# Kernel optimization log

Hardware: AMD Instinct MI355X
Metric: run time of the kernel (lower is better)

Reference implementation:

```python
import jax, jax.numpy as jnp
import numpy as np

N, E, DIN, DOUT = 40000, 640000, 128, 10


def _gat_layer(h_in, src, dst, W, a_src, a_dst, b, n_nodes):
    # h: [N, D]; edges include self-loops already
    h = h_in @ W
    alpha = jax.nn.leaky_relu((h @ a_src)[src] + (h @ a_dst)[dst], 0.2)  # [E']
    m = jax.ops.segment_max(alpha, dst, num_segments=n_nodes)
    e = jnp.exp(alpha - m[dst])
    s = jax.ops.segment_sum(e, dst, num_segments=n_nodes)
    coef = e / (s[dst] + 1e-16)
    out = jax.ops.segment_sum(h[src] * coef[:, None], dst, num_segments=n_nodes)
    return out + b


def setup_inputs() -> dict:
    key = jax.random.key(0)
    ks = jax.random.split(key, 20)
    p = lambda k, shp: (jax.random.normal(k, shp, dtype=jnp.float32) * 0.05)
    inp = {
        "x": jax.random.normal(ks[0], (N, DIN), dtype=jnp.float32),
        "edge_index": jax.random.randint(ks[1], (2, E), 0, N, dtype=jnp.int32),
        "batch": jnp.sort(jax.random.randint(ks[2], (N,), 0, 64, dtype=jnp.int32)),
        "edge_attr": jax.random.normal(ks[3], (E, 4), dtype=jnp.float32),
        # GATConv 1: 128 -> 64
        "W1": p(ks[4], (DIN, 64)), "a1s": p(ks[5], (64,)), "a1d": p(ks[6], (64,)), "b1": jnp.zeros((64,), jnp.float32),
        # GATConv 2: 64 -> 128
        "W2": p(ks[7], (64, 128)), "a2s": p(ks[8], (128,)), "a2d": p(ks[9], (128,)), "b2": jnp.zeros((128,), jnp.float32),
        # GATConv 3: 128 -> 128
        "W3": p(ks[10], (128, 128)), "a3s": p(ks[11], (128,)), "a3d": p(ks[12], (128,)), "b3": jnp.zeros((128,), jnp.float32),
        # SAGPooling scorer: GraphConv(128, 1)
        "wp_rel": p(ks[13], (128, 1)), "wp_root": p(ks[14], (128, 1)), "bp": jnp.zeros((1,), jnp.float32),
        # final Linear(128, out_channels)
        "Wl": p(ks[15], (128, DOUT)), "bl": jnp.zeros((DOUT,), jnp.float32),
    }
    return inp


def reference(x, edge_index, batch, edge_attr,
              W1, a1s, a1d, b1, W2, a2s, a2d, b2, W3, a3s, a3d, b3,
              wp_rel, wp_root, bp, Wl, bl):
    n = x.shape[0]
    src, dst = edge_index[0], edge_index[1]
    # GATConv adds self-loops (edge_attr unused: edge_dim=None)
    loops = jnp.arange(n, dtype=src.dtype)
    src_sl = jnp.concatenate([src, loops])
    dst_sl = jnp.concatenate([dst, loops])

    h = jax.nn.relu(_gat_layer(x, src_sl, dst_sl, W1, a1s, a1d, b1, n))
    h = jax.nn.relu(_gat_layer(h, src_sl, dst_sl, W2, a2s, a2d, b2, n))
    h = jax.nn.relu(_gat_layer(h, src_sl, dst_sl, W3, a3s, a3d, b3, n))

    # SAGPooling(ratio=1): score via GraphConv (no self-loops), tanh gating, all nodes kept
    agg = jax.ops.segment_sum(h[src], dst, num_segments=n)  # [N, 128]
    score = (agg @ wp_rel + h @ wp_root + bp)[:, 0]         # [N]
    h = h * jnp.tanh(score)[:, None]

    # dropout is identity in eval mode
    return jax.nn.relu(h @ Wl + bl)
```

## Files before the change

### kernel.cpp

```cpp
#include <hip/hip_runtime.h>
#include <math.h>

template<int K, int N>
__global__ __launch_bounds__(128) void gemm_rt(
    const float* __restrict__ A, const float* __restrict__ B,
    float* __restrict__ C, int M,
    const float* __restrict__ va, const float* __restrict__ vb,
    float* __restrict__ outa, float* __restrict__ outb)
{
    constexpr int KC = 32;
    constexpr int NC = K / KC;
    constexpr int TC = N / 8;
    constexpr int TR = 128 / TC;
    constexpr int MR = 64 / TR;
    constexpr int KT = KC / TC;
    constexpr int AST = 68;

    __shared__ float AsT[KC * AST];
    __shared__ float Bs[KC * N];

    const int tid = threadIdx.x;
    const int base = blockIdx.x * 64;
    const int tc = tid % TC;
    const int tr = tid / TC;
    const int sq = tid & 7;
    const int sr = tid >> 3;

    float acc[MR][8];
#pragma unroll
    for (int m = 0; m < MR; ++m)
#pragma unroll
        for (int j = 0; j < 8; ++j) acc[m][j] = 0.f;
    float sa[MR], sb[MR];
#pragma unroll
    for (int m = 0; m < MR; ++m) { sa[m] = 0.f; sb[m] = 0.f; }

    for (int ch = 0; ch < NC; ++ch) {
        const int k0 = ch * KC;
#pragma unroll
        for (int rr = sr; rr < 64; rr += 16) {
            int gr = base + rr;
            float4 av = (gr < M) ? *(const float4*)(A + (size_t)gr * K + k0 + 4 * sq)
                                 : make_float4(0.f, 0.f, 0.f, 0.f);
            AsT[(4 * sq + 0) * AST + rr] = av.x;
            AsT[(4 * sq + 1) * AST + rr] = av.y;
            AsT[(4 * sq + 2) * AST + rr] = av.z;
            AsT[(4 * sq + 3) * AST + rr] = av.w;
        }
#pragma unroll
        for (int t = tid; t < KC * N / 4; t += 128) {
            int f = t * 4;
            int k = f / N, c = f % N;
            *(float4*)(Bs + k * N + c) = *(const float4*)(B + (size_t)(k0 + k) * N + c);
        }
        __syncthreads();

#pragma unroll 4
        for (int kk = 0; kk < KC; ++kk) {
            const float* ap = AsT + kk * AST + MR * tr;
            const float* bp = Bs + kk * N + 8 * tc;
            float4 b0 = *(const float4*)(bp);
            float4 b1 = *(const float4*)(bp + 4);
            float4 a0 = *(const float4*)(ap);
#pragma unroll
            for (int m = 0; m < 4; ++m) {
                float av = ((const float*)&a0)[m];
                acc[m][0] = fmaf(av, b0.x, acc[m][0]);
                acc[m][1] = fmaf(av, b0.y, acc[m][1]);
                acc[m][2] = fmaf(av, b0.z, acc[m][2]);
                acc[m][3] = fmaf(av, b0.w, acc[m][3]);
                acc[m][4] = fmaf(av, b1.x, acc[m][4]);
                acc[m][5] = fmaf(av, b1.y, acc[m][5]);
                acc[m][6] = fmaf(av, b1.z, acc[m][6]);
                acc[m][7] = fmaf(av, b1.w, acc[m][7]);
            }
            if constexpr (MR == 8) {
                float4 a1 = *(const float4*)(ap + 4);
#pragma unroll
                for (int m = 0; m < 4; ++m) {
                    float av = ((const float*)&a1)[m];
                    acc[m + 4][0] = fmaf(av, b0.x, acc[m + 4][0]);
                    acc[m + 4][1] = fmaf(av, b0.y, acc[m + 4][1]);
                    acc[m + 4][2] = fmaf(av, b0.z, acc[m + 4][2]);
                    acc[m + 4][3] = fmaf(av, b0.w, acc[m + 4][3]);
                    acc[m + 4][4] = fmaf(av, b1.x, acc[m + 4][4]);
                    acc[m + 4][5] = fmaf(av, b1.y, acc[m + 4][5]);
                    acc[m + 4][6] = fmaf(av, b1.z, acc[m + 4][6]);
                    acc[m + 4][7] = fmaf(av, b1.w, acc[m + 4][7]);
                }
            }
        }
        if (va != nullptr) {
#pragma unroll
            for (int kl = 0; kl < KT; ++kl) {
                int k = tc * KT + kl;
                float av_ = va[k0 + k];
                float bv_ = vb[k0 + k];
#pragma unroll
                for (int m = 0; m < MR; ++m) {
                    float aval = AsT[k * AST + MR * tr + m];
                    sa[m] = fmaf(aval, av_, sa[m]);
                    sb[m] = fmaf(aval, bv_, sb[m]);
                }
            }
        }
        __syncthreads();
    }

#pragma unroll
    for (int m = 0; m < MR; ++m) {
        int gr = base + MR * tr + m;
        if (gr < M) {
            float4 o0 = make_float4(acc[m][0], acc[m][1], acc[m][2], acc[m][3]);
            float4 o1 = make_float4(acc[m][4], acc[m][5], acc[m][6], acc[m][7]);
            *(float4*)(C + (size_t)gr * N + 8 * tc) = o0;
            *(float4*)(C + (size_t)gr * N + 8 * tc + 4) = o1;
        }
    }
    if (va != nullptr) {
#pragma unroll
        for (int m = 0; m < MR; ++m) {
#pragma unroll
            for (int off = TC / 2; off; off >>= 1) {
                sa[m] += __shfl_xor(sa[m], off);
                sb[m] += __shfl_xor(sb[m], off);
            }
        }
        if (tc == 0) {
#pragma unroll
            for (int m = 0; m < MR; ++m) {
                int gr = base + MR * tr + m;
                if (gr < M) { outa[gr] = sa[m]; outb[gr] = sb[m]; }
            }
        }
    }
}

template<int K, int N, int NT>
__global__ __launch_bounds__(256) void gemm_tile(
    const float* __restrict__ A, const float* __restrict__ B,
    float* __restrict__ C, int M,
    const float* __restrict__ bias, const float* __restrict__ score, int outN)
{
    __shared__ float As[64 * K];
    const int tid = threadIdx.x;
    const int base = blockIdx.x * 64;
    for (int idx = tid; idx < 64 * K; idx += 256) {
        int r = idx / K, k = idx - r * K;
        int gr = base + r;
        As[idx] = (gr < M) ? A[(size_t)gr * K + k] : 0.f;
    }
    __syncthreads();
    constexpr int RSTEP = 256 / NT;
    constexpr int NR = 64 / RSTEP;
    const int c = tid % NT;
    const int r0 = tid / NT;
    float acc[NR];
#pragma unroll
    for (int i = 0; i < NR; ++i) acc[i] = 0.f;
    const float4* As4 = reinterpret_cast<const float4*>(As);
    const float* Bc = B + c;
    float b0 = Bc[0 * N], b1 = Bc[1 * N], b2 = Bc[2 * N], b3 = Bc[3 * N];
    for (int k = 0; k < K; k += 4) {
        const int kn = (k + 4 < K) ? (k + 4) : k;
        float n0 = Bc[(kn + 0) * N];
        float n1 = Bc[(kn + 1) * N];
        float n2 = Bc[(kn + 2) * N];
        float n3 = Bc[(kn + 3) * N];
#pragma unroll
        for (int i = 0; i < NR; ++i) {
            float4 a = As4[((r0 + i * RSTEP) * K + k) >> 2];
            acc[i] = fmaf(a.x, b0, acc[i]);
            acc[i] = fmaf(a.y, b1, acc[i]);
            acc[i] = fmaf(a.z, b2, acc[i]);
            acc[i] = fmaf(a.w, b3, acc[i]);
        }
        b0 = n0; b1 = n1; b2 = n2; b3 = n3;
    }
    if (c < outN) {
#pragma unroll
        for (int i = 0; i < NR; ++i) {
            int gr = base + r0 + i * RSTEP;
            if (gr < M) {
                float v = tanhf(score[gr]) * acc[i] + bias[c];
                C[(size_t)gr * outN + c] = fmaxf(v, 0.f);
            }
        }
    }
}

__global__ __launch_bounds__(256) void hist_deg(
    const int* __restrict__ dst, int* __restrict__ deg, int E, int n)
{
    int e = blockIdx.x * 256 + threadIdx.x;
    if (e >= E + n) return;
    int d = (e < E) ? dst[e] : (e - E);
    atomicAdd(deg + d, 1);
}

__global__ __launch_bounds__(256) void scan_local(
    const int* __restrict__ deg, int* __restrict__ row_start, int* __restrict__ blocksum, int n)
{
    __shared__ int s[256];
    const int t = threadIdx.x;
    const int i = blockIdx.x * 256 + t;
    int v = (i < n) ? deg[i] : 0;
    s[t] = v;
    __syncthreads();
#pragma unroll
    for (int off = 1; off < 256; off <<= 1) {
        int u = (t >= off) ? s[t - off] : 0;
        __syncthreads();
        s[t] += u;
        __syncthreads();
    }
    if (i < n) row_start[i] = s[t] - v;
    if (t == 255) blocksum[blockIdx.x] = s[255];
}

__global__ __launch_bounds__(256) void scan_blocks(int* __restrict__ blocksum, int nb)
{
    __shared__ int s[256];
    const int t = threadIdx.x;
    int v = (t < nb) ? blocksum[t] : 0;
    s[t] = v;
    __syncthreads();
#pragma unroll
    for (int off = 1; off < 256; off <<= 1) {
        int u = (t >= off) ? s[t - off] : 0;
        __syncthreads();
        s[t] += u;
        __syncthreads();
    }
    if (t < nb) blocksum[t] = s[t] - v;
}

__global__ __launch_bounds__(256) void scan_add(
    int* __restrict__ row_start, int* __restrict__ cursor,
    const int* __restrict__ blocksum, int n, int total)
{
    const int i = blockIdx.x * 256 + threadIdx.x;
    if (i < n) {
        int v = row_start[i] + blocksum[blockIdx.x];
        row_start[i] = v;
        cursor[i] = v;
    } else if (i == n) {
        row_start[n] = total;
    }
}

__global__ __launch_bounds__(256) void fill_csr(
    const int* __restrict__ src, const int* __restrict__ dst,
    int* __restrict__ cursor, int* __restrict__ csr_src, int E, int n)
{
    int e = blockIdx.x * 256 + threadIdx.x;
    if (e >= E + n) return;
    int s, d;
    if (e < E) { s = src[e]; d = dst[e]; } else { s = d = e - E; }
    int pos = atomicAdd(cursor + d, 1);
    csr_src[pos] = s;
}

template<int D, bool POOL>
__global__ __launch_bounds__(256) void gat_aggregate(
    const int* __restrict__ row_start, const int* __restrict__ csr_src,
    const float* __restrict__ asv, const float* __restrict__ adv,
    const float* __restrict__ h, const float* __restrict__ bias,
    float* __restrict__ out,
    const float* __restrict__ wpr, const float* __restrict__ wpo,
    float* __restrict__ poolA, float* __restrict__ poolB, int n)
{
    __shared__ float lds_e[4][128];
    __shared__ int   lds_i[4][128];
    const int node = (blockIdx.x * 256 + threadIdx.x) >> 6;
    const int lane = threadIdx.x & 63;
    const int w = threadIdx.x >> 6;
    if (node >= n) return;
    const int beg = row_start[node];
    const int deg = row_start[node + 1] - beg;
    const float advv = adv[node];
    const bool fast = (deg <= 128);

    float amax = -INFINITY;
    if (fast) {
        for (int j = lane; j < deg; j += 64) {
            int s = csr_src[beg + j];
            lds_i[w][j] = s;
            float a = asv[s] + advv;
            a = (a >= 0.f) ? a : 0.2f * a;
            lds_e[w][j] = a;
            amax = fmaxf(amax, a);
        }
    } else {
        for (int j = lane; j < deg; j += 64) {
            float a = asv[csr_src[beg + j]] + advv;
            a = (a >= 0.f) ? a : 0.2f * a;
            amax = fmaxf(amax, a);
        }
    }
#pragma unroll
    for (int off = 32; off; off >>= 1) amax = fmaxf(amax, __shfl_xor(amax, off));

    float ssum = 0.f;
    if (fast) {
        for (int j = lane; j < deg; j += 64) {
            float ev = expf(lds_e[w][j] - amax);
            lds_e[w][j] = ev;
            ssum += ev;
        }
    } else {
        for (int j = lane; j < deg; j += 64) {
            float a = asv[csr_src[beg + j]] + advv;
            a = (a >= 0.f) ? a : 0.2f * a;
            ssum += expf(a - amax);
        }
    }
#pragma unroll
    for (int off = 32; off; off >>= 1) ssum += __shfl_xor(ssum, off);
    const float inv = 1.f / (ssum + 1e-16f);

    if (fast) {
        if constexpr (D == 128) {
            const float4* h4 = reinterpret_cast<const float4*>(h);
            const int half = lane >> 5;
            const int fl = lane & 31;
            float4 a0 = {0,0,0,0}, a1 = {0,0,0,0}, a2 = {0,0,0,0}, a3 = {0,0,0,0};
            int j = 0;
            for (; j + 8 <= deg; j += 8) {
                int e0 = j + half, e1 = j + 2 + half, e2 = j + 4 + half, e3 = j + 6 + half;
                int s0 = lds_i[w][e0], s1 = lds_i[w][e1], s2 = lds_i[w][e2], s3 = lds_i[w][e3];
                float c0 = lds_e[w][e0] * inv, c1 = lds_e[w][e1] * inv;
                float c2 = lds_e[w][e2] * inv, c3 = lds_e[w][e3] * inv;
                float4 v0 = h4[(size_t)s0 * 32 + fl];
                float4 v1 = h4[(size_t)s1 * 32 + fl];
                float4 v2 = h4[(size_t)s2 * 32 + fl];
                float4 v3 = h4[(size_t)s3 * 32 + fl];
                a0.x = fmaf(v0.x, c0, a0.x); a0.y = fmaf(v0.y, c0, a0.y);
                a0.z = fmaf(v0.z, c0, a0.z); a0.w = fmaf(v0.w, c0, a0.w);
                a1.x = fmaf(v1.x, c1, a1.x); a1.y = fmaf(v1.y, c1, a1.y);
                a1.z = fmaf(v1.z, c1, a1.z); a1.w = fmaf(v1.w, c1, a1.w);
                a2.x = fmaf(v2.x, c2, a2.x); a2.y = fmaf(v2.y, c2, a2.y);
                a2.z = fmaf(v2.z, c2, a2.z); a2.w = fmaf(v2.w, c2, a2.w);
                a3.x = fmaf(v3.x, c3, a3.x); a3.y = fmaf(v3.y, c3, a3.y);
                a3.z = fmaf(v3.z, c3, a3.z); a3.w = fmaf(v3.w, c3, a3.w);
            }
            for (; j < deg; j += 2) {
                int e = j + half;
                bool ok = (e < deg);
                int s = lds_i[w][ok ? e : 0];
                float c = ok ? lds_e[w][e] * inv : 0.f;
                float4 v = h4[(size_t)s * 32 + fl];
                a0.x = fmaf(v.x, c, a0.x); a0.y = fmaf(v.y, c, a0.y);
                a0.z = fmaf(v.z, c, a0.z); a0.w = fmaf(v.w, c, a0.w);
            }
            float4 t;
            t.x = (a0.x + a1.x) + (a2.x + a3.x);
            t.y = (a0.y + a1.y) + (a2.y + a3.y);
            t.z = (a0.z + a1.z) + (a2.z + a3.z);
            t.w = (a0.w + a1.w) + (a2.w + a3.w);
            t.x += __shfl_xor(t.x, 32);
            t.y += __shfl_xor(t.y, 32);
            t.z += __shfl_xor(t.z, 32);
            t.w += __shfl_xor(t.w, 32);
            const float4 b4 = reinterpret_cast<const float4*>(bias)[fl];
            float4 o;
            o.x = fmaxf(t.x + b4.x, 0.f);
            o.y = fmaxf(t.y + b4.y, 0.f);
            o.z = fmaxf(t.z + b4.z, 0.f);
            o.w = fmaxf(t.w + b4.w, 0.f);
            if (half == 0)
                reinterpret_cast<float4*>(out)[(size_t)node * 32 + fl] = o;
            if constexpr (POOL) {
                const float4 r4 = reinterpret_cast<const float4*>(wpr)[fl];
                const float4 q4 = reinterpret_cast<const float4*>(wpo)[fl];
                float pa = o.x * r4.x + o.y * r4.y + o.z * r4.z + o.w * r4.w;
                float pb = o.x * q4.x + o.y * q4.y + o.z * q4.z + o.w * q4.w;
#pragma unroll
                for (int off = 16; off; off >>= 1) {
                    pa += __shfl_xor(pa, off);
                    pb += __shfl_xor(pb, off);
                }
                if (lane == 0) { poolA[node] = pa; poolB[node] = pb; }
            }
        } else {
            const float4* h4 = reinterpret_cast<const float4*>(h);
            const int q = lane >> 4;
            const int fl = lane & 15;
            float4 a0 = {0,0,0,0}, a1 = {0,0,0,0};
            int j = 0;
            for (; j + 8 <= deg; j += 8) {
                int e0 = j + q, e1 = j + 4 + q;
                int s0 = lds_i[w][e0], s1 = lds_i[w][e1];
                float c0 = lds_e[w][e0] * inv, c1 = lds_e[w][e1] * inv;
                float4 v0 = h4[(size_t)s0 * 16 + fl];
                float4 v1 = h4[(size_t)s1 * 16 + fl];
                a0.x = fmaf(v0.x, c0, a0.x); a0.y = fmaf(v0.y, c0, a0.y);
                a0.z = fmaf(v0.z, c0, a0.z); a0.w = fmaf(v0.w, c0, a0.w);
                a1.x = fmaf(v1.x, c1, a1.x); a1.y = fmaf(v1.y, c1, a1.y);
                a1.z = fmaf(v1.z, c1, a1.z); a1.w = fmaf(v1.w, c1, a1.w);
            }
            for (; j < deg; j += 4) {
                int e = j + q;
                bool ok = (e < deg);
                int s = lds_i[w][ok ? e : 0];
                float c = ok ? lds_e[w][e] * inv : 0.f;
                float4 v = h4[(size_t)s * 16 + fl];
                a0.x = fmaf(v.x, c, a0.x); a0.y = fmaf(v.y, c, a0.y);
                a0.z = fmaf(v.z, c, a0.z); a0.w = fmaf(v.w, c, a0.w);
            }
            float4 t;
            t.x = a0.x + a1.x; t.y = a0.y + a1.y; t.z = a0.z + a1.z; t.w = a0.w + a1.w;
            t.x += __shfl_xor(t.x, 16); t.x += __shfl_xor(t.x, 32);
            t.y += __shfl_xor(t.y, 16); t.y += __shfl_xor(t.y, 32);
            t.z += __shfl_xor(t.z, 16); t.z += __shfl_xor(t.z, 32);
            t.w += __shfl_xor(t.w, 16); t.w += __shfl_xor(t.w, 32);
            const float4 b4 = reinterpret_cast<const float4*>(bias)[fl];
            float4 o;
            o.x = fmaxf(t.x + b4.x, 0.f);
            o.y = fmaxf(t.y + b4.y, 0.f);
            o.z = fmaxf(t.z + b4.z, 0.f);
            o.w = fmaxf(t.w + b4.w, 0.f);
            if (q == 0)
                reinterpret_cast<float4*>(out)[(size_t)node * 16 + fl] = o;
        }
    } else {
        if constexpr (D == 128) {
            const float2* h2 = reinterpret_cast<const float2*>(h);
            float2 a0 = {0.f, 0.f};
            for (int j = 0; j < deg; ++j) {
                int s = csr_src[beg + j];
                float a = asv[s] + advv;
                a = (a >= 0.f) ? a : 0.2f * a;
                float c = expf(a - amax) * inv;
                float2 v = h2[(size_t)s * 64 + lane];
                a0.x = fmaf(v.x, c, a0.x); a0.y = fmaf(v.y, c, a0.y);
            }
            float2 o;
            o.x = fmaxf(a0.x + bias[2 * lane], 0.f);
            o.y = fmaxf(a0.y + bias[2 * lane + 1], 0.f);
            reinterpret_cast<float2*>(out)[(size_t)node * 64 + lane] = o;
            if constexpr (POOL) {
                float pa = fmaf(o.x, wpr[2 * lane], o.y * wpr[2 * lane + 1]);
                float pb = fmaf(o.x, wpo[2 * lane], o.y * wpo[2 * lane + 1]);
#pragma unroll
                for (int off = 32; off; off >>= 1) {
                    pa += __shfl_xor(pa, off);
                    pb += __shfl_xor(pb, off);
                }
                if (lane == 0) { poolA[node] = pa; poolB[node] = pb; }
            }
        } else {
            float a0 = 0.f;
            for (int j = 0; j < deg; ++j) {
                int s = csr_src[beg + j];
                float a = asv[s] + advv;
                a = (a >= 0.f) ? a : 0.2f * a;
                float c = expf(a - amax) * inv;
                a0 = fmaf(h[(size_t)s * D + lane], c, a0);
            }
            out[(size_t)node * D + lane] = fmaxf(a0 + bias[lane], 0.f);
        }
    }
}

__global__ __launch_bounds__(256) void score_csr(
    const int* __restrict__ row_start, const int* __restrict__ csr_src,
    const float* __restrict__ ts, const float* __restrict__ td,
    const float* __restrict__ bp, float* __restrict__ score, int n)
{
    int i = blockIdx.x * 256 + threadIdx.x;
    if (i >= n) return;
    int beg = row_start[i], end = row_start[i + 1];
    float s = td[i] + bp[0] - ts[i];
    for (int j = beg; j < end; ++j) s += ts[csr_src[j]];
    score[i] = s;
}

__global__ __launch_bounds__(256) void precompute(
    const float* __restrict__ W1, const float* __restrict__ a1s, const float* __restrict__ a1d,
    const float* __restrict__ W2, const float* __restrict__ a2s, const float* __restrict__ a2d,
    const float* __restrict__ W3, const float* __restrict__ a3s, const float* __restrict__ a3d,
    const float* __restrict__ Wl, const float* __restrict__ bl,
    float* __restrict__ va1, float* __restrict__ vb1,
    float* __restrict__ va2, float* __restrict__ vb2,
    float* __restrict__ va3, float* __restrict__ vb3,
    float* __restrict__ Wlp, float* __restrict__ blp,
    int* __restrict__ deg, int n)
{
    int t = blockIdx.x * 256 + threadIdx.x;
    if (t < n) deg[t] = 0;
    if (t < 128) {
        float sa = 0.f, sb = 0.f;
        for (int j = 0; j < 64; ++j) {
            float w = W1[t * 64 + j];
            sa = fmaf(w, a1s[j], sa); sb = fmaf(w, a1d[j], sb);
        }
        va1[t] = sa; vb1[t] = sb;
    } else if (t < 192) {
        int k = t - 128;
        float sa = 0.f, sb = 0.f;
        for (int j = 0; j < 128; ++j) {
            float w = W2[k * 128 + j];
            sa = fmaf(w, a2s[j], sa); sb = fmaf(w, a2d[j], sb);
        }
        va2[k] = sa; vb2[k] = sb;
    } else if (t < 320) {
        int k = t - 192;
        float sa = 0.f, sb = 0.f;
        for (int j = 0; j < 128; ++j) {
            float w = W3[k * 128 + j];
            sa = fmaf(w, a3s[j], sa); sb = fmaf(w, a3d[j], sb);
        }
        va3[k] = sa; vb3[k] = sb;
    } else if (t < 320 + 2048) {
        int i = t - 320;
        int k = i >> 4, c = i & 15;
        Wlp[i] = (c < 10) ? Wl[k * 10 + c] : 0.f;
    } else if (t < 320 + 2048 + 16) {
        int c = t - (320 + 2048);
        blp[c] = (c < 10) ? bl[c] : 0.f;
    }
}

extern "C" void kernel_launch(void* const* d_in, const int* in_sizes, int n_in,
                              void* d_out, int out_size, void* d_ws, size_t ws_size,
                              hipStream_t stream) {
    const float* x   = (const float*)d_in[0];
    const int*   ei  = (const int*)d_in[1];
    const float* W1  = (const float*)d_in[4];
    const float* a1s = (const float*)d_in[5];
    const float* a1d = (const float*)d_in[6];
    const float* b1  = (const float*)d_in[7];
    const float* W2  = (const float*)d_in[8];
    const float* a2s = (const float*)d_in[9];
    const float* a2d = (const float*)d_in[10];
    const float* b2  = (const float*)d_in[11];
    const float* W3  = (const float*)d_in[12];
    const float* a3s = (const float*)d_in[13];
    const float* a3d = (const float*)d_in[14];
    const float* b3  = (const float*)d_in[15];
    const float* wpr = (const float*)d_in[16];
    const float* wpo = (const float*)d_in[17];
    const float* bp  = (const float*)d_in[18];
    const float* Wl  = (const float*)d_in[19];
    const float* bl  = (const float*)d_in[20];

    const int n = in_sizes[0] / 128;
    const int E = in_sizes[1] / 2;
    const int Esl = E + n;
    const int* src = ei;
    const int* dst = ei + E;

    float* ws = (float*)d_ws;
    const size_t nd = (size_t)n * 128;
    float* bufA      = ws;
    float* bufB      = bufA + nd;
    float* asv       = bufB + nd;
    float* adv       = asv + n;
    float* tsv       = adv + n;
    float* tdv       = tsv + n;
    float* score     = tdv + n;
    int*   deg       = (int*)(score + n);
    int*   row_start = deg + n;
    int*   cursor    = row_start + n + 1;
    int*   blocksum  = cursor + n;
    int*   csr_src   = blocksum + 256;
    float* va1       = (float*)(csr_src + Esl);
    float* vb1       = va1 + 128;
    float* va2       = vb1 + 128;
    float* vb2       = va2 + 64;
    float* va3       = vb2 + 64;
    float* vb3       = va3 + 128;
    float* Wlp       = vb3 + 128;
    float* blp       = Wlp + 128 * 16;

    const unsigned EB = (unsigned)((Esl + 255) / 256);
    const unsigned NB = (unsigned)((n + 255) / 256);
    const unsigned MB = (unsigned)((n + 63) / 64);
    const unsigned WB = (unsigned)(((size_t)n * 64 + 255) / 256);

    precompute<<<NB, 256, 0, stream>>>(W1, a1s, a1d, W2, a2s, a2d, W3, a3s, a3d, Wl, bl,
                                       va1, vb1, va2, vb2, va3, vb3, Wlp, blp, deg, n);
    hist_deg<<<EB, 256, 0, stream>>>(dst, deg, E, n);
    scan_local<<<NB, 256, 0, stream>>>(deg, row_start, blocksum, n);
    scan_blocks<<<1, 256, 0, stream>>>(blocksum, (int)NB);
    scan_add<<<NB, 256, 0, stream>>>(row_start, cursor, blocksum, n, Esl);
    fill_csr<<<EB, 256, 0, stream>>>(src, dst, cursor, csr_src, E, n);

    gemm_rt<128, 64><<<MB, 128, 0, stream>>>(x, W1, bufA, n, va1, vb1, asv, adv);
    gat_aggregate<64, false><<<WB, 256, 0, stream>>>(row_start, csr_src, asv, adv, bufA, b1, bufB,
                                                     nullptr, nullptr, nullptr, nullptr, n);

    gemm_rt<64, 128><<<MB, 128, 0, stream>>>(bufB, W2, bufA, n, va2, vb2, asv, adv);
    gat_aggregate<128, false><<<WB, 256, 0, stream>>>(row_start, csr_src, asv, adv, bufA, b2, bufB,
                                                      nullptr, nullptr, nullptr, nullptr, n);

    gemm_rt<128, 128><<<MB, 128, 0, stream>>>(bufB, W3, bufA, n, va3, vb3, asv, adv);
    gat_aggregate<128, true><<<WB, 256, 0, stream>>>(row_start, csr_src, asv, adv, bufA, b3, bufB,
                                                     wpr, wpo, tsv, tdv, n);

    score_csr<<<NB, 256, 0, stream>>>(row_start, csr_src, tsv, tdv, bp, score, n);
    gemm_tile<128, 16, 16><<<MB, 256, 0, stream>>>(bufB, Wlp, (float*)d_out, n, blp, score, 10);
}
```

Measured before the change: 332.0 us.

## Register-prefetch next K-chunk in gemm_rt and scale threads with output width

```diff
diff --git a/kernel.cpp b/kernel.cpp
--- a/kernel.cpp
+++ b/kernel.cpp
@@ -2,19 +2,23 @@
 #include <math.h>
 
 template<int K, int N>
-__global__ __launch_bounds__(128) void gemm_rt(
+__global__ __launch_bounds__(2 * N) void gemm_rt(
     const float* __restrict__ A, const float* __restrict__ B,
     float* __restrict__ C, int M,
-    const float* __restrict__ va, const float* __restrict__ vb,
-    float* __restrict__ outa, float* __restrict__ outb)
+    const float* __restrict__ iva, const float* __restrict__ ivb,
+    float* __restrict__ ioa, float* __restrict__ iob,
+    const float* __restrict__ ebias,
+    const float* __restrict__ eva, const float* __restrict__ evb,
+    float* __restrict__ eoa, float* __restrict__ eob)
 {
     constexpr int KC = 32;
     constexpr int NC = K / KC;
     constexpr int TC = N / 8;
-    constexpr int TR = 128 / TC;
-    constexpr int MR = 64 / TR;
+    constexpr int NT = 2 * N;
     constexpr int KT = KC / TC;
     constexpr int AST = 68;
+    constexpr int A_F4 = 512 / NT;
+    constexpr int B_F4 = 4;
 
     __shared__ float AsT[KC * AST];
     __shared__ float Bs[KC * N];
@@ -23,45 +27,69 @@
     const int base = blockIdx.x * 64;
     const int tc = tid % TC;
     const int tr = tid / TC;
-    const int sq = tid & 7;
-    const int sr = tid >> 3;
-
-    float acc[MR][8];
-#pragma unroll
-    for (int m = 0; m < MR; ++m)
+
+    float acc[4][8];
+#pragma unroll
+    for (int m = 0; m < 4; ++m)
 #pragma unroll
         for (int j = 0; j < 8; ++j) acc[m][j] = 0.f;
-    float sa[MR], sb[MR];
-#pragma unroll
-    for (int m = 0; m < MR; ++m) { sa[m] = 0.f; sb[m] = 0.f; }
+    float sa[4], sb[4];
+#pragma unroll
+    for (int m = 0; m < 4; ++m) { sa[m] = 0.f; sb[m] = 0.f; }
+
+    float4 ra[A_F4], rb[B_F4];
+
+#pragma unroll
+    for (int j = 0; j < A_F4; ++j) {
+        int i = tid + j * NT; int row = i >> 3; int q = i & 7;
+        int gr = base + row;
+        ra[j] = (gr < M) ? *(const float4*)(A + (size_t)gr * K + 4 * q)
+                         : make_float4(0.f, 0.f, 0.f, 0.f);
+    }
+#pragma unroll
+    for (int j = 0; j < B_F4; ++j) {
+        int i = tid + j * NT; int kk_ = i / (N / 4); int c4 = i % (N / 4);
+        rb[j] = *(const float4*)(B + (size_t)kk_ * N + 4 * c4);
+    }
 
     for (int ch = 0; ch < NC; ++ch) {
-        const int k0 = ch * KC;
-#pragma unroll
-        for (int rr = sr; rr < 64; rr += 16) {
-            int gr = base + rr;
-            float4 av = (gr < M) ? *(const float4*)(A + (size_t)gr * K + k0 + 4 * sq)
+#pragma unroll
+        for (int j = 0; j < A_F4; ++j) {
+            int i = tid + j * NT; int row = i >> 3; int q = i & 7;
+            AsT[(4 * q + 0) * AST + row] = ra[j].x;
+            AsT[(4 * q + 1) * AST + row] = ra[j].y;
+            AsT[(4 * q + 2) * AST + row] = ra[j].z;
+            AsT[(4 * q + 3) * AST + row] = ra[j].w;
+        }
+#pragma unroll
+        for (int j = 0; j < B_F4; ++j) {
+            int i = tid + j * NT; int kk_ = i / (N / 4); int c4 = i % (N / 4);
+            *(float4*)(Bs + kk_ * N + 4 * c4) = rb[j];
+        }
+        __syncthreads();
+
+        if (ch + 1 < NC) {
+            const int k0 = (ch + 1) * KC;
+#pragma unroll
+            for (int j = 0; j < A_F4; ++j) {
+                int i = tid + j * NT; int row = i >> 3; int q = i & 7;
+                int gr = base + row;
+                ra[j] = (gr < M) ? *(const float4*)(A + (size_t)gr * K + k0 + 4 * q)
                                  : make_float4(0.f, 0.f, 0.f, 0.f);
-            AsT[(4 * sq + 0) * AST + rr] = av.x;
-            AsT[(4 * sq + 1) * AST + rr] = av.y;
-            AsT[(4 * sq + 2) * AST + rr] = av.z;
-            AsT[(4 * sq + 3) * AST + rr] = av.w;
-        }
-#pragma unroll
-        for (int t = tid; t < KC * N / 4; t += 128) {
-            int f = t * 4;
-            int k = f / N, c = f % N;
-            *(float4*)(Bs + k * N + c) = *(const float4*)(B + (size_t)(k0 + k) * N + c);
-        }
-        __syncthreads();
-
-#pragma unroll 4
+            }
+#pragma unroll
+            for (int j = 0; j < B_F4; ++j) {
+                int i = tid + j * NT; int kk_ = i / (N / 4); int c4 = i % (N / 4);
+                rb[j] = *(const float4*)(B + (size_t)(k0 + kk_) * N + 4 * c4);
+            }
+        }
+
+#pragma unroll 8
         for (int kk = 0; kk < KC; ++kk) {
-            const float* ap = AsT + kk * AST + MR * tr;
+            float4 a0 = *(const float4*)(AsT + kk * AST + 4 * tr);
             const float* bp = Bs + kk * N + 8 * tc;
             float4 b0 = *(const float4*)(bp);
             float4 b1 = *(const float4*)(bp + 4);
-            float4 a0 = *(const float4*)(ap);
 #pragma unroll
             for (int m = 0; m < 4; ++m) {
                 float av = ((const float*)&a0)[m];
@@ -74,31 +102,18 @@
                 acc[m][6] = fmaf(av, b1.z, acc[m][6]);
                 acc[m][7] = fmaf(av, b1.w, acc[m][7]);
             }
-            if constexpr (MR == 8) {
-                float4 a1 = *(const float4*)(ap + 4);
-#pragma unroll
-                for (int m = 0; m < 4; ++m) {
-                    float av = ((const float*)&a1)[m];
-                    acc[m + 4][0] = fmaf(av, b0.x, acc[m + 4][0]);
-                    acc[m + 4][1] = fmaf(av, b0.y, acc[m + 4][1]);
-                    acc[m + 4][2] = fmaf(av, b0.z, acc[m + 4][2]);
-                    acc[m + 4][3] = fmaf(av, b0.w, acc[m + 4][3]);
-                    acc[m + 4][4] = fmaf(av, b1.x, acc[m + 4][4]);
-                    acc[m + 4][5] = fmaf(av, b1.y, acc[m + 4][5]);
-                    acc[m + 4][6] = fmaf(av, b1.z, acc[m + 4][6]);
-                    acc[m + 4][7] = fmaf(av, b1.w, acc[m + 4][7]);
-                }
-            }
-        }
-        if (va != nullptr) {
+        }
+
+        if (iva != nullptr) {
+            const int k0 = ch * KC;
 #pragma unroll
             for (int kl = 0; kl < KT; ++kl) {
                 int k = tc * KT + kl;
-                float av_ = va[k0 + k];
-                float bv_ = vb[k0 + k];
-#pragma unroll
-                for (int m = 0; m < MR; ++m) {
-                    float aval = AsT[k * AST + MR * tr + m];
+                float av_ = iva[k0 + k];
+                float bv_ = ivb[k0 + k];
+#pragma unroll
+                for (int m = 0; m < 4; ++m) {
+                    float aval = AsT[k * AST + 4 * tr + m];
                     sa[m] = fmaf(aval, av_, sa[m]);
                     sb[m] = fmaf(aval, bv_, sb[m]);
                 }
@@ -107,19 +122,51 @@
         __syncthreads();
     }
 
-#pragma unroll
-    for (int m = 0; m < MR; ++m) {
-        int gr = base + MR * tr + m;
+    float pa[4], pb[4];
+#pragma unroll
+    for (int m = 0; m < 4; ++m) { pa[m] = 0.f; pb[m] = 0.f; }
+#pragma unroll
+    for (int m = 0; m < 4; ++m) {
+        int gr = base + 4 * tr + m;
+        float o[8];
+#pragma unroll
+        for (int j = 0; j < 8; ++j) o[j] = acc[m][j];
+        if (ebias != nullptr) {
+#pragma unroll
+            for (int j = 0; j < 8; ++j) o[j] = fmaxf(o[j] + ebias[8 * tc + j], 0.f);
+        }
         if (gr < M) {
-            float4 o0 = make_float4(acc[m][0], acc[m][1], acc[m][2], acc[m][3]);
-            float4 o1 = make_float4(acc[m][4], acc[m][5], acc[m][6], acc[m][7]);
-            *(float4*)(C + (size_t)gr * N + 8 * tc) = o0;
-            *(float4*)(C + (size_t)gr * N + 8 * tc + 4) = o1;
-        }
-    }
-    if (va != nullptr) {
-#pragma unroll
-        for (int m = 0; m < MR; ++m) {
+            *(float4*)(C + (size_t)gr * N + 8 * tc) = make_float4(o[0], o[1], o[2], o[3]);
+            *(float4*)(C + (size_t)gr * N + 8 * tc + 4) = make_float4(o[4], o[5], o[6], o[7]);
+        }
+        if (eva != nullptr) {
+#pragma unroll
+            for (int j = 0; j < 8; ++j) {
+                pa[m] = fmaf(o[j], eva[8 * tc + j], pa[m]);
+                pb[m] = fmaf(o[j], evb[8 * tc + j], pb[m]);
+            }
+        }
+    }
+    if (eva != nullptr) {
+#pragma unroll
+        for (int m = 0; m < 4; ++m) {
+#pragma unroll
+            for (int off = TC / 2; off; off >>= 1) {
+                pa[m] += __shfl_xor(pa[m], off);
+                pb[m] += __shfl_xor(pb[m], off);
+            }
+        }
+        if (tc == 0) {
+#pragma unroll
+            for (int m = 0; m < 4; ++m) {
+                int gr = base + 4 * tr + m;
+                if (gr < M) { eoa[gr] = pa[m]; eob[gr] = pb[m]; }
+            }
+        }
+    }
+    if (iva != nullptr) {
+#pragma unroll
+        for (int m = 0; m < 4; ++m) {
 #pragma unroll
             for (int off = TC / 2; off; off >>= 1) {
                 sa[m] += __shfl_xor(sa[m], off);
@@ -128,9 +175,9 @@
         }
         if (tc == 0) {
 #pragma unroll
-            for (int m = 0; m < MR; ++m) {
-                int gr = base + MR * tr + m;
-                if (gr < M) { outa[gr] = sa[m]; outb[gr] = sb[m]; }
+            for (int m = 0; m < 4; ++m) {
+                int gr = base + 4 * tr + m;
+                if (gr < M) { ioa[gr] = sa[m]; iob[gr] = sb[m]; }
             }
         }
     }
@@ -587,15 +634,18 @@
     scan_add<<<NB, 256, 0, stream>>>(row_start, cursor, blocksum, n, Esl);
     fill_csr<<<EB, 256, 0, stream>>>(src, dst, cursor, csr_src, E, n);
 
-    gemm_rt<128, 64><<<MB, 128, 0, stream>>>(x, W1, bufA, n, va1, vb1, asv, adv);
+    gemm_rt<128, 64><<<MB, 128, 0, stream>>>(
+        x, W1, bufA, n, va1, vb1, asv, adv, nullptr, nullptr, nullptr, nullptr, nullptr);
     gat_aggregate<64, false><<<WB, 256, 0, stream>>>(row_start, csr_src, asv, adv, bufA, b1, bufB,
                                                      nullptr, nullptr, nullptr, nullptr, n);
 
-    gemm_rt<64, 128><<<MB, 128, 0, stream>>>(bufB, W2, bufA, n, va2, vb2, asv, adv);
+    gemm_rt<64, 128><<<MB, 256, 0, stream>>>(
+        bufB, W2, bufA, n, va2, vb2, asv, adv, nullptr, nullptr, nullptr, nullptr, nullptr);
     gat_aggregate<128, false><<<WB, 256, 0, stream>>>(row_start, csr_src, asv, adv, bufA, b2, bufB,
                                                       nullptr, nullptr, nullptr, nullptr, n);
 
-    gemm_rt<128, 128><<<MB, 128, 0, stream>>>(bufB, W3, bufA, n, va3, vb3, asv, adv);
+    gemm_rt<128, 128><<<MB, 256, 0, stream>>>(
+        bufB, W3, bufA, n, va3, vb3, asv, adv, nullptr, nullptr, nullptr, nullptr, nullptr);
     gat_aggregate<128, true><<<WB, 256, 0, stream>>>(row_start, csr_src, asv, adv, bufA, b3, bufB,
                                                      wpr, wpo, tsv, tdv, n);
 
```

Result: faster. 308.5 us (-7.1%).
